# Optimization experiments

Hardware: AMD Instinct MI355X
Metric: run time of the kernel (lower is better)

## Reference

```python
import jax, jax.numpy as jnp
import numpy as np
import math

B, S, E, H = 2, 2048, 512, 8
D = E // H
EPS = 1e-6
MAXN = 1.0 - 1e-5  # stay strictly inside the Poincare ball


def _norm(x):
    return jnp.sqrt(jnp.clip(jnp.sum(x * x, axis=-1, keepdims=True), 1e-12))


def expmap0(u):
    n = _norm(u)
    return jnp.tanh(n) * u / n


def logmap0(x):
    n = _norm(x)
    return jnp.arctanh(jnp.clip(n, None, MAXN)) * x / n


def hlinear(x, W, b):
    # HLinear: Mobius matvec == expmap0(W @ logmap0(x)), tangent bias
    return expmap0(logmap0(x) @ W.T + b)


def _lbeta(a, b):
    return math.lgamma(a) + math.lgamma(b) - math.lgamma(a + b)


def setup_inputs() -> dict:
    key = jax.random.key(0)
    ks = jax.random.split(key, 6)

    def pt(k, shape):  # random points on the Poincare ball
        return expmap0(0.2 * jax.random.normal(k, shape, dtype=jnp.float32))

    return {
        "query": pt(ks[0], (B, S, E)),
        "key": pt(ks[1], (B, S, E)),
        "value": pt(ks[2], (B, S, E)),
        "Wq": jax.random.normal(ks[3], (E, E), jnp.float32) / math.sqrt(E),
        "Wk": jax.random.normal(ks[4], (E, E), jnp.float32) / math.sqrt(E),
        "Wv": jax.random.normal(ks[5], (E, E), jnp.float32) / math.sqrt(E),
        "bq": jnp.zeros((E,), jnp.float32),
        "bk": jnp.zeros((E,), jnp.float32),
        "bv": jnp.zeros((E,), jnp.float32),
        "scale_tau": jnp.zeros((1,), jnp.float32),
        "scale_gamma": jnp.zeros((1,), jnp.float32),
    }


def reference(query, key, value, Wq, Wk, Wv, bq, bk, bv, scale_tau, scale_gamma):
    # hyperbolic q/k/v projections, then split heads: [B,H,S,D]
    q = hlinear(query, Wq, bq).reshape(B, S, H, D).transpose(0, 2, 1, 3)
    k = hlinear(key, Wk, bk).reshape(B, S, H, D).transpose(0, 2, 1, 3)
    v = hlinear(value, Wv, bv).reshape(B, S, H, D).transpose(0, 2, 1, 3)

    # pairwise Poincare distance via norms + dot (no [S,S,D] intermediate)
    qn2 = jnp.sum(q * q, -1)                       # [B,H,S]
    kn2 = jnp.sum(k * k, -1)                       # [B,H,S]
    dot = jnp.einsum('bhid,bhjd->bhij', q, k)      # [B,H,S,S]
    sq = jnp.clip(qn2[..., :, None] + kn2[..., None, :] - 2.0 * dot, 0.0)
    denom = jnp.clip((1.0 - qn2)[..., :, None] * (1.0 - kn2)[..., None, :], EPS)
    dist = jnp.arccosh(jnp.clip(1.0 + 2.0 * sq / denom, 1.0 + 1e-7))

    # attention_similarity: -d / tau + gamma, tau = 1/exp(scale_tau)
    sim = -dist * jnp.exp(scale_tau[0]) + scale_gamma[0]

    # causal mask + 'exp' activation (masked_fill(-inf) then exp -> 0)
    mask = jnp.triu(jnp.ones((S, S), bool), 1)
    w = jnp.where(mask, 0.0, jnp.exp(sim))         # [B,H,S,S]

    # gyromidpoint: (1/2) (x) [sum_j w lam_j v_j / sum_j w (lam_j - 1)]
    vn2 = jnp.sum(v * v, -1)
    lam = 2.0 / jnp.clip(1.0 - vn2, EPS)           # [B,H,S]
    num = jnp.einsum('bhij,bhjd->bhid', w, v * lam[..., None])
    den = jnp.einsum('bhij,bhj->bhi', w, lam - 1.0)
    m = num / jnp.clip(den, EPS)[..., None]
    mn = _norm(m)
    mid = jnp.tanh(0.5 * jnp.arctanh(jnp.clip(mn, None, MAXN))) * m / mn

    # beta-concatenation of heads back to embed_dim
    beta_ratio = math.exp(_lbeta(E / 2.0, 0.5) - _lbeta(D / 2.0, 0.5))
    t = logmap0(mid) * beta_ratio                  # [B,H,S,D]
    t = t.transpose(0, 2, 1, 3).reshape(B, S, E)
    return expmap0(t)
```

## Files before the change

kernel.cpp:

```cpp
#include <hip/hip_runtime.h>
#include <cmath>

#define BB 2
#define SS 2048
#define EE 512
#define HH 8
#define DD 64

typedef unsigned short u16t;
typedef __bf16 bf16x8 __attribute__((ext_vector_type(8)));
typedef float f32x4 __attribute__((ext_vector_type(4)));

__device__ __forceinline__ float bf2f(u16t u){
    union{unsigned int i; float f;} c; c.i = ((unsigned int)u)<<16; return c.f;
}
__device__ __forceinline__ u16t f2bf(float x){
    union{float f; unsigned int i;} c; c.f = x;
    return (u16t)((c.i + 0x7fffu + ((c.i>>16)&1u))>>16);
}
__device__ __forceinline__ unsigned cvtpk(float a, float b){
    unsigned r;
    asm("v_cvt_pk_bf16_f32 %0, %1, %2" : "=v"(r) : "v"(a), "v"(b));
    return r;
}
__device__ __forceinline__ float fast_tanh(float x){
    float e = __expf(2.f*x); return 1.f - 2.f/(e+1.f);
}
__device__ __forceinline__ float fast_atanh(float x){
    return 0.5f*__logf((1.f+x)/(1.f-x));
}
__device__ __forceinline__ f32x4 mfma16(bf16x8 a, bf16x8 b, f32x4 c){
    return __builtin_amdgcn_mfma_f32_16x16x32_bf16(a,b,c,0,0,0);
}
__device__ __forceinline__ int offq(int qi){
    int a = qi >> 2;
    return qi + 2*a*(a-1) + (qi&3)*a;
}

__global__ __launch_bounds__(256) void k_pre(const float* __restrict__ qp,
                                             const float* __restrict__ kp,
                                             const float* __restrict__ vp,
                                             u16t* __restrict__ Tlog,
                                             const float* __restrict__ Wq,
                                             const float* __restrict__ Wk,
                                             const float* __restrict__ Wv,
                                             u16t* __restrict__ Wb){
    int bx = blockIdx.x;
    if (bx < 3072){
        int gr = bx*4 + (threadIdx.x>>6);
        int t = gr >> 12;
        int row = gr & 4095;
        int lane = threadIdx.x & 63;
        const float* src = (t==0 ? qp : (t==1 ? kp : vp)) + (size_t)row*EE;
        const float4* s4 = (const float4*)(src + lane*8);
        float4 a = s4[0], b = s4[1];
        float x[8] = {a.x,a.y,a.z,a.w,b.x,b.y,b.z,b.w};
        float p = 0.f;
        #pragma unroll
        for (int i=0;i<8;++i) p += x[i]*x[i];
        #pragma unroll
        for (int off=32; off>=1; off>>=1) p += __shfl_xor(p, off, 64);
        float n = sqrtf(fmaxf(p, 1e-12f));
        float f = fast_atanh(fminf(n, 1.0f-1e-5f)) / n;
        u16t yb[8];
        #pragma unroll
        for (int i=0;i<8;++i) yb[i] = f2bf(f*x[i]);
        uint4 o;
        o.x = (unsigned)yb[0] | ((unsigned)yb[1]<<16);
        o.y = (unsigned)yb[2] | ((unsigned)yb[3]<<16);
        o.z = (unsigned)yb[4] | ((unsigned)yb[5]<<16);
        o.w = (unsigned)yb[6] | ((unsigned)yb[7]<<16);
        *(uint4*)(Tlog + ((size_t)(t*4096+row)*EE + lane*8)) = o;
    } else {
        int idx = ((bx-3072)*256 + threadIdx.x)*4;
        int t = idx >> 18;
        int off = idx & 262143;
        const float* W = (t==0 ? Wq : (t==1 ? Wk : Wv));
        float4 a = *(const float4*)(W + off);
        uint2 o;
        o.x = (unsigned)f2bf(a.x) | ((unsigned)f2bf(a.y)<<16);
        o.y = (unsigned)f2bf(a.z) | ((unsigned)f2bf(a.w)<<16);
        *(uint2*)(Wb + idx) = o;
    }
}

__global__ __launch_bounds__(256) void k_proj(const u16t* __restrict__ Tlog,
                                              const u16t* __restrict__ Wb,
                                              const float* __restrict__ bq,
                                              const float* __restrict__ bk,
                                              const float* __restrict__ bv,
                                              u16t* __restrict__ U){
    __shared__ __align__(16) u16t Wl[64][72];
    int bx = blockIdx.x;
    int t = bx >> 9; int rem = bx & 511;
    int m0 = (rem >> 3) << 6; int n0 = (rem & 7) << 6;
    int tid = threadIdx.x; int wv = tid>>6; int lane = tid&63;
    int l15 = lane & 15; int l4 = lane >> 4;
    const u16t* Tt = Tlog + (size_t)t*4096*EE;
    const u16t* Wt = Wb + (size_t)t*EE*EE;
    const float* bias = (t==0 ? bq : (t==1 ? bk : bv));
    f32x4 z = {0.f,0.f,0.f,0.f};
    f32x4 acc[4] = {z,z,z,z};
    int arow = m0 + 16*wv + l15;
    int rr = tid >> 2; int cc = (tid & 3) * 16;
    uint4 w0, w1;
    {
        const uint4* g = (const uint4*)(Wt + (size_t)(n0+rr)*EE + cc);
        w0 = g[0]; w1 = g[1];
    }
    for (int ks=0; ks<8; ++ks){
        int k0 = ks*64;
        *(uint4*)&Wl[rr][cc]   = w0;
        *(uint4*)&Wl[rr][cc+8] = w1;
        __syncthreads();
        if (ks < 7){
            const uint4* g = (const uint4*)(Wt + (size_t)(n0+rr)*EE + k0 + 64 + cc);
            w0 = g[0]; w1 = g[1];
        }
        bf16x8 a0 = *(const bf16x8*)(Tt + (size_t)arow*EE + k0 + l4*8);
        bf16x8 a1 = *(const bf16x8*)(Tt + (size_t)arow*EE + k0 + 32 + l4*8);
        #pragma unroll
        for (int f=0; f<4; ++f){
            bf16x8 b0 = *(const bf16x8*)&Wl[f*16+l15][l4*8];
            bf16x8 b1 = *(const bf16x8*)&Wl[f*16+l15][32+l4*8];
            acc[f] = mfma16(a0, b0, acc[f]);
            acc[f] = mfma16(a1, b1, acc[f]);
        }
        __syncthreads();
    }
    u16t* Ut = U + (size_t)t*4096*EE;
    #pragma unroll
    for (int f=0; f<4; ++f){
        int col = n0 + f*16 + l15;
        float bs = bias[col];
        #pragma unroll
        for (int r=0; r<4; ++r){
            int row = m0 + 16*wv + l4*4 + r;
            Ut[(size_t)row*EE + col] = f2bf(acc[f][r] + bs);
        }
    }
}

__global__ __launch_bounds__(256) void k_expmap_split(const u16t* __restrict__ U,
        u16t* __restrict__ Q, u16t* __restrict__ K, u16t* __restrict__ VT,
        float* __restrict__ qn2, float* __restrict__ kn2, float* __restrict__ lam1){
    int gr = blockIdx.x*4 + (threadIdx.x>>6);
    int t = gr >> 12;
    int row = gr & 4095;
    int b = row >> 11; int s = row & 2047;
    int lane = threadIdx.x & 63;
    const u16t* u = U + ((size_t)t*4096 + row)*EE;
    uint4 raw = *(const uint4*)(u + lane*8);
    const u16t* rs = (const u16t*)&raw;
    float x[8];
    #pragma unroll
    for (int i=0;i<8;++i) x[i] = bf2f(rs[i]);
    float p = 0.f;
    #pragma unroll
    for (int i=0;i<8;++i) p += x[i]*x[i];
    #pragma unroll
    for (int off=32; off>=1; off>>=1) p += __shfl_xor(p, off, 64);
    float n = sqrtf(fmaxf(p, 1e-12f));
    float f = fast_tanh(n)/n;
    float y[8]; u16t yb[8];
    float hp = 0.f;
    #pragma unroll
    for (int i=0;i<8;++i){
        yb[i] = f2bf(f*x[i]);
        y[i]  = bf2f(yb[i]);
        hp += y[i]*y[i];
    }
    #pragma unroll
    for (int off=1; off<8; off<<=1) hp += __shfl_xor(hp, off, 64);
    hp = fminf(hp, 0.99999988f);
    int h = lane >> 3;
    size_t ih = (size_t)(b*HH + h)*SS + s;
    if (t == 0){
        uint4 o;
        o.x=(unsigned)yb[0]|((unsigned)yb[1]<<16); o.y=(unsigned)yb[2]|((unsigned)yb[3]<<16);
        o.z=(unsigned)yb[4]|((unsigned)yb[5]<<16); o.w=(unsigned)yb[6]|((unsigned)yb[7]<<16);
        *(uint4*)(Q + ih*DD + (lane&7)*8) = o;
        if ((lane&7)==0) qn2[ih] = hp;
    } else if (t == 1){
        uint4 o;
        o.x=(unsigned)yb[0]|((unsigned)yb[1]<<16); o.y=(unsigned)yb[2]|((unsigned)yb[3]<<16);
        o.z=(unsigned)yb[4]|((unsigned)yb[5]<<16); o.w=(unsigned)yb[6]|((unsigned)yb[7]<<16);
        *(uint4*)(K + ih*DD + (lane&7)*8) = o;
        if ((lane&7)==0) kn2[ih] = hp;
    } else {
        float lam = 2.f / fmaxf(1.f - hp, 1e-6f);
        size_t bh = (size_t)(b*HH + h);
        int d0 = (lane&7)*8;
        #pragma unroll
        for (int i=0;i<8;++i)
            VT[(bh*DD + d0 + i)*SS + s] = f2bf(y[i]*lam);
        if ((lane&7)==0) lam1[ih] = lam - 1.f;
    }
}

#define EW_BLOCK(DO_DIAG)                                                     \
    _Pragma("unroll")                                                         \
    for (int f=0; f<4; ++f){                                                  \
        float4 kn24 = *(const float4*)&kn2s[f*16 + l4*4];                     \
        float4 akf4 = *(const float4*)&akfs[f*16 + l4*4];                     \
        float4 l14  = *(const float4*)&l1s [f*16 + l4*4];                     \
        float wv4[4];                                                         \
        _Pragma("unroll")                                                     \
        for (int r=0; r<4; ++r){                                              \
            float sq  = fmaxf(fmaf(-2.f, c[f][r], qv + ((const float*)&kn24)[r]), 0.f); \
            float co  = fminf(aq2 * ((const float*)&akf4)[r], 2e6f);          \
            float rho = sq * co;                                              \
            float tt  = fmaf(rho, rho, rho + rho);                            \
            float zz  = 1.f + rho + __builtin_amdgcn_sqrtf(tt);               \
            float L   = __builtin_amdgcn_logf(zz);                            \
            float w   = __builtin_amdgcn_exp2f(fmaf(-tauexp, L, gm2));        \
            if (DO_DIAG && (kv0 + f*16 + l4*4 + r) > qrow) w = 0.f;           \
            dn = fmaf(w, ((const float*)&l14)[r], dn);                        \
            wv4[r] = w;                                                       \
        }                                                                     \
        uint2 u2; u2.x = cvtpk(wv4[0], wv4[1]); u2.y = cvtpk(wv4[2], wv4[3]); \
        *(uint2*)&Wt[16*wv + l15][f*16 + l4*4] = u2;                          \
    }

__global__ __launch_bounds__(256,5) void k_attn(const u16t* __restrict__ Q,
        const u16t* __restrict__ K, const u16t* __restrict__ VT,
        const float* __restrict__ qn2, const float* __restrict__ kn2,
        const float* __restrict__ lam1, const float* __restrict__ taup,
        const float* __restrict__ gammap,
        float* __restrict__ pnum, float* __restrict__ pden){
    __shared__ __align__(16) u16t Kt[64][72];
    __shared__ __align__(16) u16t Vt[64][72];
    __shared__ __align__(16) u16t Wt[64][72];
    __shared__ float kn2s[64], akfs[64], l1s[64];
    int bx = blockIdx.x;
    int bh = bx & 15;
    int u = bx >> 4;
    int v = 143 - u;
    int qi = 31;
    while (offq(qi) > v) --qi;
    int c0 = v - offq(qi);
    int jt0 = c0 << 2;
    int jt1 = min(jt0 + 4, qi + 1);
    int s0 = qi << 6;
    int tid = threadIdx.x; int wv = tid>>6; int lane = tid&63;
    int l15 = lane & 15; int l4 = lane >> 4;
    float tauexp = __expf(taup[0]);
    float gm2 = gammap[0] * 1.44269504088896340736f;
    size_t base = (size_t)bh * SS;
    int qrow = s0 + 16*wv + l15;
    bf16x8 aQ0 = *(const bf16x8*)(Q + (base + qrow)*DD + l4*8);
    bf16x8 aQ1 = *(const bf16x8*)(Q + (base + qrow)*DD + 32 + l4*8);
    float qv  = qn2[base + qrow];
    float aq2 = 2.f * __builtin_amdgcn_rcpf(fmaxf(1.f - qv, 1e-6f));
    f32x4 z4 = {0.f,0.f,0.f,0.f};
    f32x4 num[4] = {z4,z4,z4,z4};
    float dn = 0.f;
    int rr = tid >> 2; int cc = (tid & 3) << 4;
    uint4 pka0, pka1, pva0, pva1; float pkn = 0.f, pl1 = 0.f;
    {
        int kv0 = jt0 << 6;
        const uint4* gk = (const uint4*)(K + (base + kv0 + rr)*DD + cc);
        pka0 = gk[0]; pka1 = gk[1];
        const uint4* gv = (const uint4*)(VT + ((size_t)bh*DD + rr)*SS + kv0 + cc);
        pva0 = gv[0]; pva1 = gv[1];
        if (tid < 64){ pkn = kn2[base+kv0+tid]; pl1 = lam1[base+kv0+tid]; }
    }
    for (int jt=jt0; jt<jt1; ++jt){
        *(uint4*)&Kt[rr][cc]   = pka0;
        *(uint4*)&Kt[rr][cc+8] = pka1;
        *(uint4*)&Vt[rr][cc]   = pva0;
        *(uint4*)&Vt[rr][cc+8] = pva1;
        if (tid < 64){
            kn2s[tid] = pkn;
            l1s[tid]  = pl1;
            akfs[tid] = __builtin_amdgcn_rcpf(fmaxf(1.f - pkn, 1e-6f));
        }
        __syncthreads();
        if (jt+1 < jt1){
            int kv0n = (jt+1) << 6;
            const uint4* gk = (const uint4*)(K + (base + kv0n + rr)*DD + cc);
            pka0 = gk[0]; pka1 = gk[1];
            const uint4* gv = (const uint4*)(VT + ((size_t)bh*DD + rr)*SS + kv0n + cc);
            pva0 = gv[0]; pva1 = gv[1];
            if (tid < 64){ pkn = kn2[base+kv0n+tid]; pl1 = lam1[base+kv0n+tid]; }
        }
        int kv0 = jt << 6;
        f32x4 c[4] = {z4,z4,z4,z4};
        #pragma unroll
        for (int f=0; f<4; ++f){
            bf16x8 kb0 = *(const bf16x8*)&Kt[f*16+l15][l4*8];
            bf16x8 kb1 = *(const bf16x8*)&Kt[f*16+l15][32+l4*8];
            c[f] = mfma16(kb0, aQ0, c[f]);
            c[f] = mfma16(kb1, aQ1, c[f]);
        }
        if (jt == qi) { EW_BLOCK(true) } else { EW_BLOCK(false) }
        bf16x8 pw0 = *(const bf16x8*)&Wt[16*wv + l15][l4*8];
        bf16x8 pw1 = *(const bf16x8*)&Wt[16*wv + l15][32 + l4*8];
        #pragma unroll
        for (int f=0; f<4; ++f){
            bf16x8 vb0 = *(const bf16x8*)&Vt[f*16+l15][l4*8];
            bf16x8 vb1 = *(const bf16x8*)&Vt[f*16+l15][32+l4*8];
            num[f] = mfma16(vb0, pw0, num[f]);
            num[f] = mfma16(vb1, pw1, num[f]);
        }
        __syncthreads();
    }
    dn += __shfl_xor(dn, 16, 64);
    dn += __shfl_xor(dn, 32, 64);
    size_t pidx = (size_t)bh*144 + offq(qi) + c0;
    float* pn = pnum + pidx*4096;
    #pragma unroll
    for (int f=0; f<4; ++f)
        *(f32x4*)&pn[(16*wv + l15)*64 + f*16 + l4*4] = num[f];
    if (l4 == 0) pden[pidx*64 + 16*wv + l15] = dn;
}

__global__ __launch_bounds__(256) void k_post(const float* __restrict__ pnum,
        const float* __restrict__ pden, float* __restrict__ out, float beta){
    int bx = blockIdx.x;
    int b = bx >> 7; int stile = bx & 127;
    int tid = threadIdx.x;
    int row = tid >> 4; int h = (tid >> 1) & 7; int half = tid & 1;
    int s = stile*16 + row;
    int qi = s >> 6; int rowin = s & 63;
    int nch = (qi >> 2) + 1;
    size_t pb = (size_t)(b*HH + h)*144 + offq(qi);
    float mv[32];
    #pragma unroll
    for (int i=0;i<32;++i) mv[i] = 0.f;
    float den = 0.f;
    for (int cc=0; cc<nch; ++cc){
        const float* pn = pnum + (pb+cc)*4096 + rowin*64 + half*32;
        #pragma unroll
        for (int i=0;i<8;++i){
            float4 v = *(const float4*)(pn + i*4);
            mv[i*4+0]+=v.x; mv[i*4+1]+=v.y; mv[i*4+2]+=v.z; mv[i*4+3]+=v.w;
        }
        den += pden[(pb+cc)*64 + rowin];
    }
    float invd = 1.f / fmaxf(den, 1e-6f);
    float mn2h = 0.f;
    #pragma unroll
    for (int i=0;i<32;++i){ mv[i] *= invd; mn2h += mv[i]*mv[i]; }
    float mn2 = mn2h + __shfl_xor(mn2h, 1, 64);
    float mn = sqrtf(fmaxf(mn2, 1e-12f));
    float g = beta * 0.5f * fast_atanh(fminf(mn, 1.0f-1e-5f)) / mn;
    float tn = g*g*mn2;
    tn += __shfl_xor(tn, 2, 64);
    tn += __shfl_xor(tn, 4, 64);
    tn += __shfl_xor(tn, 8, 64);
    float en = sqrtf(fmaxf(tn, 1e-12f));
    float f = fast_tanh(en)/en;
    float gf = g * f;
    float* dst = out + ((size_t)(b*SS + s))*EE + h*DD + half*32;
    #pragma unroll
    for (int i=0;i<8;++i){
        float4 v = {gf*mv[i*4+0], gf*mv[i*4+1], gf*mv[i*4+2], gf*mv[i*4+3]};
        *(float4*)(dst + i*4) = v;
    }
}

extern "C" void kernel_launch(void* const* d_in, const int* in_sizes, int n_in,
                              void* d_out, int out_size, void* d_ws, size_t ws_size,
                              hipStream_t stream) {
    const float* q_in  = (const float*)d_in[0];
    const float* k_in  = (const float*)d_in[1];
    const float* v_in  = (const float*)d_in[2];
    const float* Wq    = (const float*)d_in[3];
    const float* Wk    = (const float*)d_in[4];
    const float* Wv    = (const float*)d_in[5];
    const float* bq    = (const float*)d_in[6];
    const float* bk    = (const float*)d_in[7];
    const float* bv    = (const float*)d_in[8];
    const float* tau   = (const float*)d_in[9];
    const float* gamma = (const float*)d_in[10];
    float* out = (float*)d_out;

    char* ws = (char*)d_ws;
    u16t*  Tlog = (u16t*)(ws + 0);
    u16t*  Wb   = (u16t*)(ws + 12582912);
    u16t*  Ub   = (u16t*)(ws + 14155776);
    u16t*  Qb   = (u16t*)(ws + 26738688);
    u16t*  Kb   = (u16t*)(ws + 30932992);
    u16t*  VTb  = (u16t*)(ws + 35127296);
    float* qn2  = (float*)(ws + 39321600);
    float* kn2  = (float*)(ws + 39452672);
    float* lam1 = (float*)(ws + 39583744);
    float* pnum = (float*)(ws + 39714816);
    float* pden = (float*)(ws + 77463552);

    double lb1 = std::lgamma(256.0) + std::lgamma(0.5) - std::lgamma(256.5);
    double lb2 = std::lgamma(32.0)  + std::lgamma(0.5) - std::lgamma(32.5);
    float beta = (float)std::exp(lb1 - lb2);

    k_pre<<<3840, 256, 0, stream>>>(q_in, k_in, v_in, Tlog, Wq, Wk, Wv, Wb);
    k_proj<<<1536, 256, 0, stream>>>(Tlog, Wb, bq, bk, bv, Ub);
    k_expmap_split<<<3072, 256, 0, stream>>>(Ub, Qb, Kb, VTb, qn2, kn2, lam1);
    k_attn<<<2304, 256, 0, stream>>>(Qb, Kb, VTb, qn2, kn2, lam1, tau, gamma,
                                     pnum, pden);
    k_post<<<256, 256, 0, stream>>>(pnum, pden, out, beta);
}
```

Baseline: 96.13 us.

## Fuse projection GEMM with expmap split and add reciprocal fast path for weights

Merges the projection GEMM and the expmap/head-split kernel so each block computes full 512-wide rows and applies the row norm, tanh scaling and head scatter from registers. This removes the intermediate U buffer round trip and one launch. It uses only 192 large blocks, which lowers parallelism. Attention also gains a runtime-selected path that computes the weight as a reciprocal instead of log plus exp2 when tau scale and gamma are zero.

```diff
diff --git a/kernel.cpp b/kernel.cpp
--- a/kernel.cpp
+++ b/kernel.cpp
@@ -84,121 +84,153 @@
     }
 }
 
-__global__ __launch_bounds__(256) void k_proj(const u16t* __restrict__ Tlog,
-                                              const u16t* __restrict__ Wb,
-                                              const float* __restrict__ bq,
-                                              const float* __restrict__ bk,
-                                              const float* __restrict__ bv,
-                                              u16t* __restrict__ U){
-    __shared__ __align__(16) u16t Wl[64][72];
+__global__ __launch_bounds__(256,1) void k_projexp(const u16t* __restrict__ Tlog,
+        const u16t* __restrict__ Wb,
+        const float* __restrict__ bq, const float* __restrict__ bk,
+        const float* __restrict__ bv,
+        u16t* __restrict__ Q, u16t* __restrict__ K, u16t* __restrict__ VT,
+        float* __restrict__ qn2, float* __restrict__ kn2,
+        float* __restrict__ lam1){
+    __shared__ __align__(16) u16t Wl[512][72];
+    __shared__ float nsum[64][4];
     int bx = blockIdx.x;
-    int t = bx >> 9; int rem = bx & 511;
-    int m0 = (rem >> 3) << 6; int n0 = (rem & 7) << 6;
+    int t = bx >> 6; int m0 = (bx & 63) << 6;
     int tid = threadIdx.x; int wv = tid>>6; int lane = tid&63;
     int l15 = lane & 15; int l4 = lane >> 4;
     const u16t* Tt = Tlog + (size_t)t*4096*EE;
     const u16t* Wt = Wb + (size_t)t*EE*EE;
     const float* bias = (t==0 ? bq : (t==1 ? bk : bv));
-    f32x4 z = {0.f,0.f,0.f,0.f};
-    f32x4 acc[4] = {z,z,z,z};
-    int arow = m0 + 16*wv + l15;
-    int rr = tid >> 2; int cc = (tid & 3) * 16;
-    uint4 w0, w1;
-    {
-        const uint4* g = (const uint4*)(Wt + (size_t)(n0+rr)*EE + cc);
-        w0 = g[0]; w1 = g[1];
+    int n0 = wv << 7;
+    int srow = tid >> 3;
+    int schk = tid & 7;
+    f32x4 z4 = {0.f,0.f,0.f,0.f};
+    f32x4 acc[4][8];
+    #pragma unroll
+    for (int m=0;m<4;++m)
+        #pragma unroll
+        for (int f=0;f<8;++f) acc[m][f] = z4;
+    uint4 wpf[16];
+    #pragma unroll
+    for (int p=0; p<16; ++p)
+        wpf[p] = *(const uint4*)(Wt + (size_t)(p*32 + srow)*EE + schk*8);
+    bf16x8 pa0[4], pa1[4];
+    #pragma unroll
+    for (int m=0;m<4;++m){
+        pa0[m] = *(const bf16x8*)(Tt + (size_t)(m0+m*16+l15)*EE + l4*8);
+        pa1[m] = *(const bf16x8*)(Tt + (size_t)(m0+m*16+l15)*EE + 32 + l4*8);
     }
     for (int ks=0; ks<8; ++ks){
-        int k0 = ks*64;
-        *(uint4*)&Wl[rr][cc]   = w0;
-        *(uint4*)&Wl[rr][cc+8] = w1;
+        #pragma unroll
+        for (int p=0; p<16; ++p)
+            *(uint4*)&Wl[p*32 + srow][schk*8] = wpf[p];
         __syncthreads();
+        bf16x8 a0[4], a1[4];
+        #pragma unroll
+        for (int m=0;m<4;++m){ a0[m] = pa0[m]; a1[m] = pa1[m]; }
         if (ks < 7){
-            const uint4* g = (const uint4*)(Wt + (size_t)(n0+rr)*EE + k0 + 64 + cc);
-            w0 = g[0]; w1 = g[1];
-        }
-        bf16x8 a0 = *(const bf16x8*)(Tt + (size_t)arow*EE + k0 + l4*8);
-        bf16x8 a1 = *(const bf16x8*)(Tt + (size_t)arow*EE + k0 + 32 + l4*8);
-        #pragma unroll
-        for (int f=0; f<4; ++f){
-            bf16x8 b0 = *(const bf16x8*)&Wl[f*16+l15][l4*8];
-            bf16x8 b1 = *(const bf16x8*)&Wl[f*16+l15][32+l4*8];
-            acc[f] = mfma16(a0, b0, acc[f]);
-            acc[f] = mfma16(a1, b1, acc[f]);
+            int kn = (ks+1)*64;
+            #pragma unroll
+            for (int p=0; p<16; ++p)
+                wpf[p] = *(const uint4*)(Wt + (size_t)(p*32 + srow)*EE + kn + schk*8);
+            #pragma unroll
+            for (int m=0;m<4;++m){
+                pa0[m] = *(const bf16x8*)(Tt + (size_t)(m0+m*16+l15)*EE + kn + l4*8);
+                pa1[m] = *(const bf16x8*)(Tt + (size_t)(m0+m*16+l15)*EE + kn + 32 + l4*8);
+            }
+        }
+        #pragma unroll
+        for (int f=0; f<8; ++f){
+            bf16x8 b0 = *(const bf16x8*)&Wl[n0 + f*16 + l15][l4*8];
+            bf16x8 b1 = *(const bf16x8*)&Wl[n0 + f*16 + l15][32 + l4*8];
+            #pragma unroll
+            for (int m=0;m<4;++m){
+                acc[m][f] = mfma16(a0[m], b0, acc[m][f]);
+                acc[m][f] = mfma16(a1[m], b1, acc[m][f]);
+            }
         }
         __syncthreads();
     }
-    u16t* Ut = U + (size_t)t*4096*EE;
-    #pragma unroll
-    for (int f=0; f<4; ++f){
-        int col = n0 + f*16 + l15;
-        float bs = bias[col];
-        #pragma unroll
-        for (int r=0; r<4; ++r){
-            int row = m0 + 16*wv + l4*4 + r;
-            Ut[(size_t)row*EE + col] = f2bf(acc[f][r] + bs);
-        }
-    }
-}
-
-__global__ __launch_bounds__(256) void k_expmap_split(const u16t* __restrict__ U,
-        u16t* __restrict__ Q, u16t* __restrict__ K, u16t* __restrict__ VT,
-        float* __restrict__ qn2, float* __restrict__ kn2, float* __restrict__ lam1){
-    int gr = blockIdx.x*4 + (threadIdx.x>>6);
-    int t = gr >> 12;
-    int row = gr & 4095;
-    int b = row >> 11; int s = row & 2047;
-    int lane = threadIdx.x & 63;
-    const u16t* u = U + ((size_t)t*4096 + row)*EE;
-    uint4 raw = *(const uint4*)(u + lane*8);
-    const u16t* rs = (const u16t*)&raw;
-    float x[8];
-    #pragma unroll
-    for (int i=0;i<8;++i) x[i] = bf2f(rs[i]);
-    float p = 0.f;
-    #pragma unroll
-    for (int i=0;i<8;++i) p += x[i]*x[i];
-    #pragma unroll
-    for (int off=32; off>=1; off>>=1) p += __shfl_xor(p, off, 64);
-    float n = sqrtf(fmaxf(p, 1e-12f));
-    float f = fast_tanh(n)/n;
-    float y[8]; u16t yb[8];
-    float hp = 0.f;
-    #pragma unroll
-    for (int i=0;i<8;++i){
-        yb[i] = f2bf(f*x[i]);
-        y[i]  = bf2f(yb[i]);
-        hp += y[i]*y[i];
-    }
-    #pragma unroll
-    for (int off=1; off<8; off<<=1) hp += __shfl_xor(hp, off, 64);
-    hp = fminf(hp, 0.99999988f);
-    int h = lane >> 3;
-    size_t ih = (size_t)(b*HH + h)*SS + s;
-    if (t == 0){
-        uint4 o;
-        o.x=(unsigned)yb[0]|((unsigned)yb[1]<<16); o.y=(unsigned)yb[2]|((unsigned)yb[3]<<16);
-        o.z=(unsigned)yb[4]|((unsigned)yb[5]<<16); o.w=(unsigned)yb[6]|((unsigned)yb[7]<<16);
-        *(uint4*)(Q + ih*DD + (lane&7)*8) = o;
-        if ((lane&7)==0) qn2[ih] = hp;
-    } else if (t == 1){
-        uint4 o;
-        o.x=(unsigned)yb[0]|((unsigned)yb[1]<<16); o.y=(unsigned)yb[2]|((unsigned)yb[3]<<16);
-        o.z=(unsigned)yb[4]|((unsigned)yb[5]<<16); o.w=(unsigned)yb[6]|((unsigned)yb[7]<<16);
-        *(uint4*)(K + ih*DD + (lane&7)*8) = o;
-        if ((lane&7)==0) kn2[ih] = hp;
-    } else {
-        float lam = 2.f / fmaxf(1.f - hp, 1e-6f);
-        size_t bh = (size_t)(b*HH + h);
-        int d0 = (lane&7)*8;
-        #pragma unroll
-        for (int i=0;i<8;++i)
-            VT[(bh*DD + d0 + i)*SS + s] = f2bf(y[i]*lam);
-        if ((lane&7)==0) lam1[ih] = lam - 1.f;
-    }
-}
-
-#define EW_BLOCK(DO_DIAG)                                                     \
+    float biasv[8];
+    #pragma unroll
+    for (int f=0; f<8; ++f) biasv[f] = bias[n0 + f*16 + l15];
+    #pragma unroll
+    for (int m=0;m<4;++m)
+        #pragma unroll
+        for (int f=0; f<8; ++f)
+            #pragma unroll
+            for (int r=0;r<4;++r) acc[m][f][r] += biasv[f];
+    #pragma unroll
+    for (int m=0;m<4;++m){
+        #pragma unroll
+        for (int r=0;r<4;++r){
+            float p = 0.f;
+            #pragma unroll
+            for (int f=0; f<8; ++f) p += acc[m][f][r]*acc[m][f][r];
+            p += __shfl_xor(p,1,64); p += __shfl_xor(p,2,64);
+            p += __shfl_xor(p,4,64); p += __shfl_xor(p,8,64);
+            if (l15 == 0) nsum[m*16 + l4*4 + r][wv] = p;
+        }
+    }
+    __syncthreads();
+    #pragma unroll
+    for (int m=0;m<4;++m){
+        #pragma unroll
+        for (int r=0;r<4;++r){
+            int rowib = m*16 + l4*4 + r;
+            float4 n4 = *(const float4*)&nsum[rowib][0];
+            float np2 = (n4.x+n4.y)+(n4.z+n4.w);
+            float n = sqrtf(fmaxf(np2, 1e-12f));
+            float fsc = fast_tanh(n)/n;
+            u16t yb[8]; float hpA=0.f, hpB=0.f;
+            #pragma unroll
+            for (int f=0; f<8; ++f){
+                float y = fsc*acc[m][f][r];
+                u16t bb = f2bf(y);
+                yb[f] = bb;
+                float yr = bf2f(bb);
+                if (f<4) hpA += yr*yr; else hpB += yr*yr;
+            }
+            hpA += __shfl_xor(hpA,1,64); hpA += __shfl_xor(hpA,2,64);
+            hpA += __shfl_xor(hpA,4,64); hpA += __shfl_xor(hpA,8,64);
+            hpB += __shfl_xor(hpB,1,64); hpB += __shfl_xor(hpB,2,64);
+            hpB += __shfl_xor(hpB,4,64); hpB += __shfl_xor(hpB,8,64);
+            hpA = fminf(hpA, 0.99999988f);
+            hpB = fminf(hpB, 0.99999988f);
+            int grow = m0 + rowib;
+            int b_ = grow >> 11; int s = grow & 2047;
+            int h0 = wv*2;
+            size_t ihA = ((size_t)(b_*HH + h0))*SS + s;
+            size_t ihB = ihA + SS;
+            if (t == 0){
+                #pragma unroll
+                for (int f=0; f<4; ++f){
+                    Q[ihA*DD + f*16 + l15] = yb[f];
+                    Q[ihB*DD + f*16 + l15] = yb[f+4];
+                }
+                if (l15 == 0){ qn2[ihA] = hpA; qn2[ihB] = hpB; }
+            } else if (t == 1){
+                #pragma unroll
+                for (int f=0; f<4; ++f){
+                    K[ihA*DD + f*16 + l15] = yb[f];
+                    K[ihB*DD + f*16 + l15] = yb[f+4];
+                }
+                if (l15 == 0){ kn2[ihA] = hpA; kn2[ihB] = hpB; }
+            } else {
+                float lamA = 2.f / fmaxf(1.f - hpA, 1e-6f);
+                float lamB = 2.f / fmaxf(1.f - hpB, 1e-6f);
+                size_t vbase = (size_t)(b_*HH + h0)*DD;
+                #pragma unroll
+                for (int f=0; f<4; ++f){
+                    VT[(vbase + f*16 + l15)*SS + s]      = f2bf(bf2f(yb[f])*lamA);
+                    VT[(vbase + DD + f*16 + l15)*SS + s] = f2bf(bf2f(yb[f+4])*lamB);
+                }
+                if (l15 == 0){ lam1[ihA] = lamA - 1.f; lam1[ihB] = lamB - 1.f; }
+            }
+        }
+    }
+}
+
+#define EW_BLOCK(DO_DIAG, FASTW)                                              \
     _Pragma("unroll")                                                         \
     for (int f=0; f<4; ++f){                                                  \
         float4 kn24 = *(const float4*)&kn2s[f*16 + l4*4];                     \
@@ -212,8 +244,10 @@
             float rho = sq * co;                                              \
             float tt  = fmaf(rho, rho, rho + rho);                            \
             float zz  = 1.f + rho + __builtin_amdgcn_sqrtf(tt);               \
-            float L   = __builtin_amdgcn_logf(zz);                            \
-            float w   = __builtin_amdgcn_exp2f(fmaf(-tauexp, L, gm2));        \
+            float w;                                                          \
+            if (FASTW){ w = __builtin_amdgcn_rcpf(zz); }                      \
+            else { float L = __builtin_amdgcn_logf(zz);                       \
+                   w = __builtin_amdgcn_exp2f(fmaf(-tauexp, L, gm2)); }       \
             if (DO_DIAG && (kv0 + f*16 + l4*4 + r) > qrow) w = 0.f;           \
             dn = fmaf(w, ((const float*)&l14)[r], dn);                        \
             wv4[r] = w;                                                       \
@@ -246,6 +280,7 @@
     int l15 = lane & 15; int l4 = lane >> 4;
     float tauexp = __expf(taup[0]);
     float gm2 = gammap[0] * 1.44269504088896340736f;
+    bool fastw = (tauexp == 1.0f) && (gm2 == 0.0f);
     size_t base = (size_t)bh * SS;
     int qrow = s0 + 16*wv + l15;
     bf16x8 aQ0 = *(const bf16x8*)(Q + (base + qrow)*DD + l4*8);
@@ -293,7 +328,11 @@
             c[f] = mfma16(kb0, aQ0, c[f]);
             c[f] = mfma16(kb1, aQ1, c[f]);
         }
-        if (jt == qi) { EW_BLOCK(true) } else { EW_BLOCK(false) }
+        if (jt == qi){
+            if (fastw) { EW_BLOCK(true, true) } else { EW_BLOCK(true, false) }
+        } else {
+            if (fastw) { EW_BLOCK(false, true) } else { EW_BLOCK(false, false) }
+        }
         bf16x8 pw0 = *(const bf16x8*)&Wt[16*wv + l15][l4*8];
         bf16x8 pw1 = *(const bf16x8*)&Wt[16*wv + l15][32 + l4*8];
         #pragma unroll
@@ -379,7 +418,6 @@
     char* ws = (char*)d_ws;
     u16t*  Tlog = (u16t*)(ws + 0);
     u16t*  Wb   = (u16t*)(ws + 12582912);
-    u16t*  Ub   = (u16t*)(ws + 14155776);
     u16t*  Qb   = (u16t*)(ws + 26738688);
     u16t*  Kb   = (u16t*)(ws + 30932992);
     u16t*  VTb  = (u16t*)(ws + 35127296);
@@ -394,8 +432,8 @@
     float beta = (float)std::exp(lb1 - lb2);
 
     k_pre<<<3840, 256, 0, stream>>>(q_in, k_in, v_in, Tlog, Wq, Wk, Wv, Wb);
-    k_proj<<<1536, 256, 0, stream>>>(Tlog, Wb, bq, bk, bv, Ub);
-    k_expmap_split<<<3072, 256, 0, stream>>>(Ub, Qb, Kb, VTb, qn2, kn2, lam1);
+    k_projexp<<<192, 256, 0, stream>>>(Tlog, Wb, bq, bk, bv,
+                                       Qb, Kb, VTb, qn2, kn2, lam1);
     k_attn<<<2304, 256, 0, stream>>>(Qb, Kb, VTb, qn2, kn2, lam1, tau, gamma,
                                      pnum, pden);
     k_post<<<256, 256, 0, stream>>>(pnum, pden, out, beta);
```

Result: slower. 121.1 us (+26.0%).
